# Kernel optimization log

Hardware: AMD Instinct MI355X
Metric: run time of the kernel (lower is better)

## Reference

```python
import jax, jax.numpy as jnp
import numpy as np

NEG_SLOPE = 0.2
EPS = 1e-16

N_NODES = 100000
N_EDGES = 1600000


def setup_inputs() -> dict:
    key = jax.random.key(0)
    ks = jax.random.split(key, 12)
    x = jax.random.normal(ks[0], (N_NODES, 4), dtype=jnp.float32)
    edge_index = jax.random.randint(ks[1], (2, N_EDGES), 0, N_NODES, dtype=jnp.int64)
    # conv1: GATConv(4, 32, heads=4)
    W1 = jax.random.normal(ks[2], (4, 4 * 32), dtype=jnp.float32) * (1.0 / np.sqrt(4))
    att_src1 = jax.random.normal(ks[3], (4, 32), dtype=jnp.float32) * 0.1
    att_dst1 = jax.random.normal(ks[4], (4, 32), dtype=jnp.float32) * 0.1
    b1 = jnp.zeros((4 * 32,), dtype=jnp.float32)
    # conv2: GATConv(128, 32, heads=1)
    W2 = jax.random.normal(ks[5], (128, 32), dtype=jnp.float32) * (1.0 / np.sqrt(128))
    att_src2 = jax.random.normal(ks[6], (1, 32), dtype=jnp.float32) * 0.1
    att_dst2 = jax.random.normal(ks[7], (1, 32), dtype=jnp.float32) * 0.1
    b2 = jnp.zeros((32,), dtype=jnp.float32)
    # lin: Linear(32, 2)
    lin_w = jax.random.normal(ks[8], (32, 2), dtype=jnp.float32) * (1.0 / np.sqrt(32))
    lin_b = jnp.zeros((2,), dtype=jnp.float32)
    return {"x": x, "edge_index": edge_index, "W1": W1, "att_src1": att_src1,
            "att_dst1": att_dst1, "b1": b1, "W2": W2, "att_src2": att_src2,
            "att_dst2": att_dst2, "b2": b2, "lin_w": lin_w, "lin_b": lin_b}


def gat_conv(x, src, dst, W, a_src, a_dst, bias, n_nodes):
    # x: [N, Fin]; W: [Fin, H*Fout]; a_src/a_dst: [H, Fout]
    H, Fout = a_src.shape
    xw = (x @ W).reshape(n_nodes, H, Fout)                      # [N, H, Fout]
    alpha_s = jnp.sum(xw * a_src[None], axis=-1)                # [N, H]
    alpha_d = jnp.sum(xw * a_dst[None], axis=-1)                # [N, H]
    e = alpha_s[src] + alpha_d[dst]                             # [E, H]
    e = jnp.where(e > 0, e, NEG_SLOPE * e)                      # leaky relu
    m = jax.ops.segment_max(e, dst, num_segments=n_nodes)      # softmax over incoming edges per target
    m = jnp.where(jnp.isfinite(m), m, 0.0)
    ex = jnp.exp(e - m[dst])
    s = jax.ops.segment_sum(ex, dst, num_segments=n_nodes)
    alpha = ex / (s[dst] + EPS)                                 # [E, H]
    msg = xw[src] * alpha[:, :, None]                           # [E, H, Fout]
    out = jax.ops.segment_sum(msg, dst, num_segments=n_nodes)  # [N, H, Fout]
    return out.reshape(n_nodes, H * Fout) + bias, alpha


def reference(x, edge_index, W1, att_src1, att_dst1, b1, W2, att_src2, att_dst2, b2, lin_w, lin_b):
    n = x.shape[0]
    # PyG GATConv default: add self loops
    loops = jnp.arange(n, dtype=edge_index.dtype)
    src = jnp.concatenate([edge_index[0], loops])
    dst = jnp.concatenate([edge_index[1], loops])
    h, _ = gat_conv(x, src, dst, W1, att_src1, att_dst1, b1, n)   # [N, 128]
    h = jax.nn.elu(h)
    h, attn = gat_conv(h, src, dst, W2, att_src2, att_dst2, b2, n)  # [N, 32], attn [E+N, 1]
    h = jax.nn.elu(h)
    pooled = jnp.mean(h, axis=0, keepdims=True)                   # [1, 32]
    logits = pooled @ lin_w + lin_b                               # [1, 2]
    return logits, attn
```

## Files before the change

### kernel.cpp

```cpp
#include <hip/hip_runtime.h>
#include <hip/hip_bf16.h>
#include <hip/hip_fp16.h>

#define NN 100000
#define NE 1600000
#define ET 1700000
#define NEG_SLOPE 0.2f
#define EPSI 1e-16f

#define SCAN_NB 98
#define DEG_PAD (SCAN_NB * 1024)

#define OFF_WF       0
#define OFF_AS1      32
#define OFF_AD1      400032
#define OFF_AS2      800032
#define OFF_ADI      900032
#define OFF_XW2H     1100032
#define OFF_OFFS     2700032
#define OFF_RANK     2800034
#define OFF_EDATA    3650034
#define OFF_POOLPART 5350036
#define OFF_DEG      5750036
#define OFF_POOL     5850388
#define OFF_BSUM     5850452
#define ZERO_START   OFF_DEG
#define ZERO_N4      ((DEG_PAD + 64) / 4)

__device__ __forceinline__ float lrelu(float v) { return v > 0.f ? v : NEG_SLOPE * v; }

__global__ void kz(float4* __restrict__ p, int n4) {
    int st = gridDim.x * 256;
    for (int i = blockIdx.x * 256 + threadIdx.x; i < n4; i += st)
        p[i] = make_float4(0.f, 0.f, 0.f, 0.f);
}

__global__ void k0_wfold(const float* __restrict__ W1, const float* __restrict__ aS1,
                         const float* __restrict__ aD1, float* __restrict__ wf) {
    int t = threadIdx.x;
    if (t < 32) {
        int u = t & 15, k = u >> 2, h = u & 3;
        const float* av = (t < 16) ? aS1 : aD1;
        float s = 0.f;
        for (int f = 0; f < 32; f++) s += W1[k * 128 + h * 32 + f] * av[h * 32 + f];
        wf[t] = s;
    }
}

__global__ void k1_att1(const float* __restrict__ x, const float* __restrict__ wf,
                        float* __restrict__ as1, float* __restrict__ ad1) {
    int n = blockIdx.x * 256 + threadIdx.x;
    if (n >= NN) return;
    float4 xv = *(const float4*)(x + n * 4);
#pragma unroll
    for (int h = 0; h < 4; h++) {
        as1[n * 4 + h] = xv.x * wf[h] + xv.y * wf[4 + h] + xv.z * wf[8 + h] + xv.w * wf[12 + h];
        ad1[n * 4 + h] = xv.x * wf[16 + h] + xv.y * wf[20 + h] + xv.z * wf[24 + h] + xv.w * wf[28 + h];
    }
}

__global__ void kc1_deg(const int* __restrict__ ei, int* __restrict__ deg,
                        unsigned short* __restrict__ rank) {
    int e = blockIdx.x * 256 + threadIdx.x;
    if (e >= ET) return;
    int d_ = (e < NE) ? ei[NE + e] : (e - NE);
    rank[e] = (unsigned short)atomicAdd(&deg[d_], 1);
}

__global__ void kc2a(const int* __restrict__ deg, int* __restrict__ bsum) {
    __shared__ int ws_[4];
    int b = blockIdx.x, t = threadIdx.x;
    int4 d = *(const int4*)(deg + b * 1024 + t * 4);
    int s = d.x + d.y + d.z + d.w;
#pragma unroll
    for (int m = 1; m < 64; m <<= 1) s += __shfl_xor(s, m);
    if ((t & 63) == 0) ws_[t >> 6] = s;
    __syncthreads();
    if (t == 0) bsum[b] = ws_[0] + ws_[1] + ws_[2] + ws_[3];
}

__global__ void kc2c(const int* __restrict__ deg, const int* __restrict__ bsum,
                     int* __restrict__ offs) {
    __shared__ int bs[128];
    __shared__ int ts[256];
    int b = blockIdx.x, t = threadIdx.x;
    if (t < 128) bs[t] = (t < SCAN_NB) ? bsum[t] : 0;
    __syncthreads();
    for (int off = 1; off < 128; off <<= 1) {
        int u = (t >= off && t < 128) ? bs[t - off] : 0;
        __syncthreads();
        if (t < 128) bs[t] += u;
        __syncthreads();
    }
    int bpre = (b == 0) ? 0 : bs[b - 1];
    int base = b * 1024 + t * 4;
    int4 d = *(const int4*)(deg + base);
    int s = d.x + d.y + d.z + d.w;
    ts[t] = s;
    __syncthreads();
    for (int off = 1; off < 256; off <<= 1) {
        int u = (t >= off) ? ts[t - off] : 0;
        __syncthreads();
        ts[t] += u;
        __syncthreads();
    }
    int r = bpre + ((t == 0) ? 0 : ts[t - 1]);
    if (base < NN)     offs[base] = r;     r += d.x;
    if (base + 1 < NN) offs[base + 1] = r; r += d.y;
    if (base + 2 < NN) offs[base + 2] = r; r += d.z;
    if (base + 3 < NN) offs[base + 3] = r;
    if (b == 0 && t == 0) offs[NN] = bs[SCAN_NB - 1];
}

__global__ void kc3_fill(const int* __restrict__ ei, const int* __restrict__ offs,
                         const unsigned short* __restrict__ rank, int* __restrict__ edata) {
    int e = blockIdx.x * 256 + threadIdx.x;
    if (e >= ET) return;
    int s_, d_;
    if (e < NE) { s_ = ei[e]; d_ = ei[NE + e]; } else { s_ = d_ = e - NE; }
    edata[offs[d_] + (int)rank[e]] = s_;
}

__global__ __launch_bounds__(256) void k4ab(
    const int* __restrict__ offs, const int* __restrict__ edata,
    const float* __restrict__ x, const float* __restrict__ as1,
    const float* __restrict__ ad1, const float* __restrict__ W1,
    const float* __restrict__ b1, const float* __restrict__ W2,
    const float* __restrict__ aw_s2, const float* __restrict__ aw_d2,
    __half* __restrict__ xw2h, float* __restrict__ as2, float* __restrict__ adi) {
    __shared__ float4 wq[32][32];
    __shared__ float hs[4][128];
    int tid = threadIdx.x;
    int wv = tid >> 6, ln = tid & 63;
    int n = blockIdx.x * 4 + wv;
    for (int idx = tid; idx < 1024; idx += 256) {
        int kq = idx >> 5, sf = idx & 31;
        int kbase = kq * 4;
        wq[kq][sf] = make_float4(W2[(kbase + 0) * 32 + sf], W2[(kbase + 1) * 32 + sf],
                                 W2[(kbase + 2) * 32 + sf], W2[(kbase + 3) * 32 + sf]);
    }
    int hq = ln & 3, p = ln >> 2;
    float ad = ad1[n * 4 + hq];
    float z0 = 0.f, z1 = 0.f, z2 = 0.f, z3 = 0.f, den = 0.f;
    int beg = offs[n], end = offs[n + 1];
    for (int j = beg + p; j < end; j += 16) {
        int src = edata[j];
        float ex = __expf(lrelu(as1[src * 4 + hq] + ad));
        float4 xv = *(const float4*)(x + src * 4);
        den += ex;
        z0 += ex * xv.x; z1 += ex * xv.y; z2 += ex * xv.z; z3 += ex * xv.w;
    }
#pragma unroll
    for (int m = 4; m <= 32; m <<= 1) {
        den += __shfl_xor(den, m);
        z0 += __shfl_xor(z0, m); z1 += __shfl_xor(z1, m);
        z2 += __shfl_xor(z2, m); z3 += __shfl_xor(z3, m);
    }
    float inv = 1.f / (den + EPSI);
    float v0 = z0 * inv, v1 = z1 * inv, v2 = z2 * inv, v3 = z3 * inv;
    int f0 = ln * 2, h = ln >> 4;
    float mx = __shfl(v0, h), my = __shfl(v1, h), mz = __shfl(v2, h), mw = __shfl(v3, h);
    float h0 = mx * W1[f0]     + my * W1[128 + f0]     + mz * W1[256 + f0]     + mw * W1[384 + f0]     + b1[f0];
    float h1 = mx * W1[f0 + 1] + my * W1[128 + f0 + 1] + mz * W1[256 + f0 + 1] + mw * W1[384 + f0 + 1] + b1[f0 + 1];
    h0 = h0 > 0.f ? h0 : (__expf(h0) - 1.f);
    h1 = h1 > 0.f ? h1 : (__expf(h1) - 1.f);
    hs[wv][f0] = h0; hs[wv][f0 + 1] = h1;
    __syncthreads();
    int f = ln & 31, kq0 = (ln >> 5) * 16;
    const float* hrow = &hs[wv][kq0 * 4];
    float a0 = 0.f, a1 = 0.f;
#pragma unroll
    for (int q = 0; q < 16; q++) {
        float4 hv  = *(const float4*)(hrow + 4 * q);
        float4 wv4 = wq[kq0 + q][f];
        a0 += hv.x * wv4.x + hv.y * wv4.y;
        a1 += hv.z * wv4.z + hv.w * wv4.w;
    }
    float a = a0 + a1;
    a += __shfl_xor(a, 32);
    float ps = a * aw_s2[f], pd = a * aw_d2[f];
#pragma unroll
    for (int m2 = 1; m2 < 32; m2 <<= 1) { ps += __shfl_xor(ps, m2); pd += __shfl_xor(pd, m2); }
    if (ln < 32) xw2h[n * 32 + f] = __float2half_rn(a);
    if (ln == 0) { as2[n] = ps; adi[2 * n] = pd; }
}

__global__ __launch_bounds__(256) void k6_conv2(
    const int* __restrict__ offs, const int* __restrict__ edata,
    const __half2* __restrict__ xw2h2, const float* __restrict__ as2,
    float* __restrict__ adi, const float* __restrict__ b2,
    float* __restrict__ pool_part) {
    __shared__ float2 psum[4][16];
    int sub = threadIdx.x >> 5, f = threadIdx.x & 31;
    int f2 = f & 15, g = f >> 4;
    int n = blockIdx.x * 8 + sub;
    float ad = adi[2 * n];
    float den = 0.f, accx = 0.f, accy = 0.f;
    int beg = offs[n], end = offs[n + 1];
    for (int base = beg; base < end; base += 32) {
        int j = base + f;
        int src = 0;
        float ex = 0.f;
        if (j < end) {
            src = edata[j];
            ex = __expf(lrelu(as2[src] + ad));
        }
        den += ex;
        int cnt = min(32, end - base);
        for (int k2 = 0; k2 < cnt; k2 += 2) {
            int ki = k2 + g;
            int   sk = __shfl(src, ki, 32);
            float ek = __shfl(ex, ki, 32);
            if (ki < cnt) {
                float2 fv = __half22float2(xw2h2[sk * 16 + f2]);
                accx += ek * fv.x;
                accy += ek * fv.y;
            }
        }
    }
#pragma unroll
    for (int m = 1; m < 32; m <<= 1) den += __shfl_xor(den, m, 32);
    float inv = 1.f / (den + EPSI);
    if (f == 0) adi[2 * n + 1] = inv;
    accx += __shfl_xor(accx, 16, 32);
    accy += __shfl_xor(accy, 16, 32);
    float vx = accx * inv + b2[2 * f2];
    float vy = accy * inv + b2[2 * f2 + 1];
    vx = vx > 0.f ? vx : (__expf(vx) - 1.f);
    vy = vy > 0.f ? vy : (__expf(vy) - 1.f);
    vx += __shfl_xor(vx, 32);
    vy += __shfl_xor(vy, 32);
    int wv = threadIdx.x >> 6;
    if ((threadIdx.x & 63) < 16) psum[wv][f2] = make_float2(vx, vy);
    __syncthreads();
    if (threadIdx.x < 16) {
        float2 a0 = psum[0][threadIdx.x], a1 = psum[1][threadIdx.x];
        float2 a2 = psum[2][threadIdx.x], a3 = psum[3][threadIdx.x];
        ((float2*)pool_part)[blockIdx.x * 16 + threadIdx.x] =
            make_float2(a0.x + a1.x + a2.x + a3.x, a0.y + a1.y + a2.y + a3.y);
    }
}

__global__ void k7_attn(const int* __restrict__ ei, const float* __restrict__ as2,
                        const float* __restrict__ adi, float* __restrict__ attn) {
    int e = blockIdx.x * 256 + threadIdx.x;
    if (e >= ET) return;
    int s_, d_;
    if (e < NE) { s_ = ei[e]; d_ = ei[NE + e]; } else { s_ = d_ = e - NE; }
    float2 av = *(const float2*)(adi + 2 * d_);
    attn[e] = __expf(lrelu(as2[s_] + av.x)) * av.y;
}

__global__ void k8_pool(const float* __restrict__ pool_part, float* __restrict__ pool) {
    int tid = threadIdx.x;
    int f = tid & 31;
    float acc = 0.f;
    int st = gridDim.x * 256;
    for (int i = blockIdx.x * 256 + tid; i < 12500 * 32; i += st) acc += pool_part[i];
    acc += __shfl_xor(acc, 32);
    if ((tid & 63) < 32) unsafeAtomicAdd(&pool[f], acc);
}

__global__ void k9_logits(const float* __restrict__ pool, const float* __restrict__ lin_w,
                          const float* __restrict__ lin_b, float* __restrict__ out) {
    int j = threadIdx.x;
    if (j < 2) {
        float s = 0.f;
        for (int f = 0; f < 32; f++) s += (pool[f] * (1.0f / NN)) * lin_w[f * 2 + j];
        out[j] = s + lin_b[j];
    }
}

extern "C" void kernel_launch(void* const* d_in, const int* in_sizes, int n_in,
                              void* d_out, int out_size, void* d_ws, size_t ws_size,
                              hipStream_t stream) {
    const float* x    = (const float*)d_in[0];
    const int*   ei   = (const int*)d_in[1];
    const float* W1   = (const float*)d_in[2];
    const float* aS1  = (const float*)d_in[3];
    const float* aD1  = (const float*)d_in[4];
    const float* b1   = (const float*)d_in[5];
    const float* W2   = (const float*)d_in[6];
    const float* aS2  = (const float*)d_in[7];
    const float* aD2  = (const float*)d_in[8];
    const float* b2   = (const float*)d_in[9];
    const float* linw = (const float*)d_in[10];
    const float* linb = (const float*)d_in[11];

    float*          ws    = (float*)d_ws;
    float*          wf    = ws + OFF_WF;
    float*          as1   = ws + OFF_AS1;
    float*          ad1   = ws + OFF_AD1;
    float*          as2   = ws + OFF_AS2;
    float*          adi   = ws + OFF_ADI;
    __half*         xw2h  = (__half*)(ws + OFF_XW2H);
    int*            offs  = (int*)(ws + OFF_OFFS);
    unsigned short* rank  = (unsigned short*)(ws + OFF_RANK);
    int*            ed    = (int*)(ws + OFF_EDATA);
    float*          ppart = ws + OFF_POOLPART;
    int*            deg   = (int*)(ws + OFF_DEG);
    float*          pool  = ws + OFF_POOL;
    int*            bsum  = (int*)(ws + OFF_BSUM);

    float* logits = (float*)d_out;
    float* attn   = (float*)d_out + 2;

    kz<<<98, 256, 0, stream>>>((float4*)(ws + ZERO_START), ZERO_N4);
    k0_wfold<<<1, 64, 0, stream>>>(W1, aS1, aD1, wf);
    k1_att1<<<(NN + 255) / 256, 256, 0, stream>>>(x, wf, as1, ad1);
    kc1_deg<<<(ET + 255) / 256, 256, 0, stream>>>(ei, deg, rank);
    kc2a<<<SCAN_NB, 256, 0, stream>>>(deg, bsum);
    kc2c<<<SCAN_NB, 256, 0, stream>>>(deg, bsum, offs);
    kc3_fill<<<(ET + 255) / 256, 256, 0, stream>>>(ei, offs, rank, ed);
    k4ab<<<NN / 4, 256, 0, stream>>>(offs, ed, x, as1, ad1, W1, b1, W2,
                                     aS2, aD2, xw2h, as2, adi);
    k6_conv2<<<NN / 8, 256, 0, stream>>>(offs, ed, (const __half2*)xw2h, as2, adi,
                                         b2, ppart);
    k7_attn<<<(ET + 255) / 256, 256, 0, stream>>>(ei, as2, adi, attn);
    k8_pool<<<256, 256, 0, stream>>>(ppart, pool);
    k9_logits<<<1, 64, 0, stream>>>(pool, linw, linb, logits);
}
```

Baseline: 273.7 us.

## Process four nodes per wavefront in fused conv1/projection kernel

The fused conv1 aggregation plus W2 projection kernel now assigns four nodes to each wavefront, with 16 lanes per node, instead of one node per wavefront. The W2 tile staged in shared memory is reused across four times as many nodes, and the grid shrinks by four. Each node's edge loop now has only 4 lanes per head instead of 16, so high-degree nodes take longer per lane, and register use grows from the four-way accumulators.

After: 353.9 us. 29.3% more time.

```diff
diff --git a/kernel.cpp b/kernel.cpp
--- a/kernel.cpp
+++ b/kernel.cpp
@@ -129,21 +129,22 @@
     const float* __restrict__ aw_s2, const float* __restrict__ aw_d2,
     __half* __restrict__ xw2h, float* __restrict__ as2, float* __restrict__ adi) {
     __shared__ float4 wq[32][32];
-    __shared__ float hs[4][128];
+    __shared__ float hsf[4][4][128];
     int tid = threadIdx.x;
     int wv = tid >> 6, ln = tid & 63;
-    int n = blockIdx.x * 4 + wv;
+    int g = ln >> 4, q16 = ln & 15, hq = q16 & 3, p = q16 >> 2;
+    int nbase = blockIdx.x * 16 + wv * 4;
+    int ng = nbase + g;
     for (int idx = tid; idx < 1024; idx += 256) {
         int kq = idx >> 5, sf = idx & 31;
-        int kbase = kq * 4;
-        wq[kq][sf] = make_float4(W2[(kbase + 0) * 32 + sf], W2[(kbase + 1) * 32 + sf],
-                                 W2[(kbase + 2) * 32 + sf], W2[(kbase + 3) * 32 + sf]);
-    }
-    int hq = ln & 3, p = ln >> 2;
-    float ad = ad1[n * 4 + hq];
+        int kb = kq * 4;
+        wq[kq][sf] = make_float4(W2[(kb + 0) * 32 + sf], W2[(kb + 1) * 32 + sf],
+                                 W2[(kb + 2) * 32 + sf], W2[(kb + 3) * 32 + sf]);
+    }
+    float ad = ad1[ng * 4 + hq];
     float z0 = 0.f, z1 = 0.f, z2 = 0.f, z3 = 0.f, den = 0.f;
-    int beg = offs[n], end = offs[n + 1];
-    for (int j = beg + p; j < end; j += 16) {
+    int beg = offs[ng], end = offs[ng + 1];
+    for (int j = beg + p; j < end; j += 4) {
         int src = edata[j];
         float ex = __expf(lrelu(as1[src * 4 + hq] + ad));
         float4 xv = *(const float4*)(x + src * 4);
@@ -151,38 +152,53 @@
         z0 += ex * xv.x; z1 += ex * xv.y; z2 += ex * xv.z; z3 += ex * xv.w;
     }
 #pragma unroll
-    for (int m = 4; m <= 32; m <<= 1) {
-        den += __shfl_xor(den, m);
-        z0 += __shfl_xor(z0, m); z1 += __shfl_xor(z1, m);
-        z2 += __shfl_xor(z2, m); z3 += __shfl_xor(z3, m);
+    for (int m = 4; m <= 8; m <<= 1) {
+        den += __shfl_xor(den, m, 16);
+        z0 += __shfl_xor(z0, m, 16); z1 += __shfl_xor(z1, m, 16);
+        z2 += __shfl_xor(z2, m, 16); z3 += __shfl_xor(z3, m, 16);
     }
     float inv = 1.f / (den + EPSI);
     float v0 = z0 * inv, v1 = z1 * inv, v2 = z2 * inv, v3 = z3 * inv;
-    int f0 = ln * 2, h = ln >> 4;
-    float mx = __shfl(v0, h), my = __shfl(v1, h), mz = __shfl(v2, h), mw = __shfl(v3, h);
-    float h0 = mx * W1[f0]     + my * W1[128 + f0]     + mz * W1[256 + f0]     + mw * W1[384 + f0]     + b1[f0];
-    float h1 = mx * W1[f0 + 1] + my * W1[128 + f0 + 1] + mz * W1[256 + f0 + 1] + mw * W1[384 + f0 + 1] + b1[f0 + 1];
-    h0 = h0 > 0.f ? h0 : (__expf(h0) - 1.f);
-    h1 = h1 > 0.f ? h1 : (__expf(h1) - 1.f);
-    hs[wv][f0] = h0; hs[wv][f0 + 1] = h1;
+    int f0 = ln * 2;
+    float w10 = W1[f0],       w11 = W1[f0 + 1];
+    float w20 = W1[128 + f0], w21 = W1[128 + f0 + 1];
+    float w30 = W1[256 + f0], w31 = W1[256 + f0 + 1];
+    float w40 = W1[384 + f0], w41 = W1[384 + f0 + 1];
+    float bb0 = b1[f0], bb1 = b1[f0 + 1];
+#pragma unroll
+    for (int i = 0; i < 4; i++) {
+        int sl = i * 16 + g;
+        float mx = __shfl(v0, sl), my = __shfl(v1, sl);
+        float mz = __shfl(v2, sl), mw = __shfl(v3, sl);
+        float h0 = mx * w10 + my * w20 + mz * w30 + mw * w40 + bb0;
+        float h1 = mx * w11 + my * w21 + mz * w31 + mw * w41 + bb1;
+        h0 = h0 > 0.f ? h0 : (__expf(h0) - 1.f);
+        h1 = h1 > 0.f ? h1 : (__expf(h1) - 1.f);
+        *(float2*)(&hsf[wv][i][f0]) = make_float2(h0, h1);
+    }
     __syncthreads();
     int f = ln & 31, kq0 = (ln >> 5) * 16;
-    const float* hrow = &hs[wv][kq0 * 4];
-    float a0 = 0.f, a1 = 0.f;
+    float a0[4] = {0.f, 0.f, 0.f, 0.f}, a1[4] = {0.f, 0.f, 0.f, 0.f};
 #pragma unroll
     for (int q = 0; q < 16; q++) {
-        float4 hv  = *(const float4*)(hrow + 4 * q);
         float4 wv4 = wq[kq0 + q][f];
-        a0 += hv.x * wv4.x + hv.y * wv4.y;
-        a1 += hv.z * wv4.z + hv.w * wv4.w;
-    }
-    float a = a0 + a1;
-    a += __shfl_xor(a, 32);
-    float ps = a * aw_s2[f], pd = a * aw_d2[f];
-#pragma unroll
-    for (int m2 = 1; m2 < 32; m2 <<= 1) { ps += __shfl_xor(ps, m2); pd += __shfl_xor(pd, m2); }
-    if (ln < 32) xw2h[n * 32 + f] = __float2half_rn(a);
-    if (ln == 0) { as2[n] = ps; adi[2 * n] = pd; }
+#pragma unroll
+        for (int i = 0; i < 4; i++) {
+            float4 hv = *(const float4*)(&hsf[wv][i][(kq0 + q) * 4]);
+            a0[i] += hv.x * wv4.x + hv.y * wv4.y;
+            a1[i] += hv.z * wv4.z + hv.w * wv4.w;
+        }
+    }
+#pragma unroll
+    for (int i = 0; i < 4; i++) {
+        float a = a0[i] + a1[i];
+        a += __shfl_xor(a, 32);
+        float ps = a * aw_s2[f], pd = a * aw_d2[f];
+#pragma unroll
+        for (int m = 1; m <= 16; m <<= 1) { ps += __shfl_xor(ps, m); pd += __shfl_xor(pd, m); }
+        if (ln < 32) xw2h[(nbase + i) * 32 + f] = __float2half_rn(a);
+        if (ln == 0) { as2[nbase + i] = ps; adi[2 * (nbase + i)] = pd; }
+    }
 }
 
 __global__ __launch_bounds__(256) void k6_conv2(
@@ -312,8 +328,8 @@
     kc2a<<<SCAN_NB, 256, 0, stream>>>(deg, bsum);
     kc2c<<<SCAN_NB, 256, 0, stream>>>(deg, bsum, offs);
     kc3_fill<<<(ET + 255) / 256, 256, 0, stream>>>(ei, offs, rank, ed);
-    k4ab<<<NN / 4, 256, 0, stream>>>(offs, ed, x, as1, ad1, W1, b1, W2,
-                                     aS2, aD2, xw2h, as2, adi);
+    k4ab<<<NN / 16, 256, 0, stream>>>(offs, ed, x, as1, ad1, W1, b1, W2,
+                                      aS2, aD2, xw2h, as2, adi);
     k6_conv2<<<NN / 8, 256, 0, stream>>>(offs, ed, (const __half2*)xw2h, as2, adi,
                                          b2, ppart);
     k7_attn<<<(ET + 255) / 256, 256, 0, stream>>>(ei, as2, adi, attn);
```
